# Kernel optimization log

Hardware: AMD Instinct MI355X
Metric: run time of the kernel (lower is better)

## Reference

```python
import jax, jax.numpy as jnp
import numpy as np

WS = 4           # window_size
NUM_HEADS = 4
LN_EPS = 1e-5


def setup_inputs() -> dict:
    key = jax.random.key(0)
    ks = jax.random.split(key, 8)
    d = 256
    s = 0.02
    return {
        "feature": jax.random.normal(ks[0], (8, d, 127, 127), dtype=jnp.float32),
        "ln_w": jnp.ones((d,), jnp.float32),
        "ln_b": jnp.zeros((d,), jnp.float32),
        "in_w": jax.random.normal(ks[1], (3 * d, d), jnp.float32) * s,
        "in_b": jnp.zeros((3 * d,), jnp.float32),
        "out_w": jax.random.normal(ks[2], (d, d), jnp.float32) * s,
        "out_b": jnp.zeros((d,), jnp.float32),
        "proj_w": jax.random.normal(ks[3], (d, d), jnp.float32) * s,
        "proj_b": jnp.zeros((d,), jnp.float32),
    }


def reference(feature, ln_w, ln_b, in_w, in_b, out_w, out_b, proj_w, proj_b):
    B, C, H, W = feature.shape
    ws = WS
    pad_h = (-H) % ws
    pad_w = (-W) % ws
    x = jnp.pad(feature, ((0, 0), (0, 0), (0, pad_h), (0, pad_w)))
    Hp, Wp = H + pad_h, W + pad_w
    nh, nw = Hp // ws, Wp // ws
    # NCHW -> NHWC -> windows [B*nh*nw, ws*ws, C]
    x = x.transpose(0, 2, 3, 1)
    win = (x.reshape(B, nh, ws, nw, ws, C)
            .transpose(0, 1, 3, 2, 4, 5)
            .reshape(-1, ws * ws, C))
    # LayerNorm (ddof=0, matches torch)
    mu = win.mean(-1, keepdims=True)
    var = win.var(-1, keepdims=True)
    xn = (win - mu) / jnp.sqrt(var + LN_EPS) * ln_w + ln_b
    # fused QKV projection, then split heads
    qkv = xn @ in_w.T + in_b
    q, k, v = jnp.split(qkv, 3, axis=-1)
    hd = C // NUM_HEADS
    def heads(t):
        return t.reshape(t.shape[0], t.shape[1], NUM_HEADS, hd).transpose(0, 2, 1, 3)
    q, k, v = heads(q), heads(k), heads(v)
    scores = jnp.einsum('bhqd,bhkd->bhqk', q, k) / np.float32(np.sqrt(hd))
    a = jax.nn.softmax(scores, axis=-1)
    o = jnp.einsum('bhqk,bhkd->bhqd', a, v)
    o = o.transpose(0, 2, 1, 3).reshape(-1, ws * ws, C)
    o = o @ out_w.T + out_b
    # residual + Linear + exact GELU
    y = win + jax.nn.gelu(o @ proj_w.T + proj_b, approximate=False)
    # windows -> NHWC, crop padding, -> NCHW
    y = (y.reshape(B, nh, nw, ws, ws, C)
          .transpose(0, 1, 3, 2, 4, 5)
          .reshape(B, Hp, Wp, C))
    return y[:, :H, :W, :].transpose(0, 3, 1, 2)
```

## Files before the change

kernel.cpp:

```cpp
#include <hip/hip_runtime.h>

typedef _Float16 f16;
typedef __attribute__((ext_vector_type(4))) _Float16 half4;
typedef __attribute__((ext_vector_type(8))) _Float16 half8;
typedef __attribute__((ext_vector_type(4))) float f32x4;
typedef unsigned short u16;

#define MFMA32(a,b,c) __builtin_amdgcn_mfma_f32_16x16x32_f16(a,b,c,0,0,0)
#define MFMA16(a,b,c) __builtin_amdgcn_mfma_f32_16x16x16f16(a,b,c,0,0,0)

#define W_IN0   0
#define W_OUT0  196608
#define W_PROJ0 262144
#define X0      327680
#define QK0     33882112ull
#define VT0     100990976ull

__global__ void k0_cast(const float* __restrict__ iw, const float* __restrict__ ow,
                        const float* __restrict__ pw, f16* __restrict__ W) {
    int i = blockIdx.x * 256 + threadIdx.x;
    if (i < 196608) W[W_IN0 + i] = (f16)iw[i];
    if (i < 16384) {
        const int s = i & 8191;
        const float* src = (i < 8192) ? ow : pw;
        f16* dst = W + ((i < 8192) ? W_OUT0 : W_PROJ0);
        const int r = s >> 5, sp = s & 31;
        const int u = sp ^ (r & 7);
        const int kc = u >> 2, gg = u & 3;
        const int c0 = kc * 32 + gg * 4;
        f32x4 v0 = *(const f32x4*)(src + r * 256 + c0);
        f32x4 v1 = *(const f32x4*)(src + r * 256 + c0 + 16);
        half8 o;
#pragma unroll
        for (int j = 0; j < 4; ++j) { o[j] = (f16)v0[j]; o[j + 4] = (f16)v1[j]; }
        *(half8*)(dst + (r >> 5) * 8192 + (r & 31) * 256 + sp * 8) = o;
    }
}

__global__ __launch_bounds__(256, 4)
void k1_pack(const float* __restrict__ feat, const float* __restrict__ lnw,
             const float* __restrict__ lnb, f16* __restrict__ X) {
    const int tid = threadIdx.x, lane = tid & 63, hh = tid >> 6;
    const int bid = blockIdx.x;
    const int jh = bid & 3, wi = (bid >> 2) & 31, bb = bid >> 7;
    const int h0 = wi * 4, w0 = jh * 32;
    const int wl4 = lane & 7, cg = lane >> 3;
    const int h = h0 + hh, wb = w0 + wl4 * 4;
    const bool hok = (h < 127);
    const bool edge = (wb + 3) >= 127;
    const size_t bbase = (size_t)bb * (256 * 127 * 127);
    const int c0 = cg * 32;
    const float* p0 = feat + bbase + (size_t)c0 * 16129 + (size_t)h * 127 + wb;

    half4 arr[32];
    float ss[4] = {0.f, 0.f, 0.f, 0.f}, qq[4] = {0.f, 0.f, 0.f, 0.f};
    if (hok && !edge) {
#pragma unroll
        for (int i = 0; i < 32; ++i) {
            f32x4 v = *(const f32x4*)(p0 + (size_t)i * 16129);
            half4 hv;
#pragma unroll
            for (int e = 0; e < 4; ++e) { ss[e] += v[e]; qq[e] += v[e] * v[e]; hv[e] = (f16)v[e]; }
            arr[i] = hv;
        }
    } else if (hok) {
#pragma unroll
        for (int i = 0; i < 32; ++i) {
            const float* pi = p0 + (size_t)i * 16129;
            half4 hv;
#pragma unroll
            for (int e = 0; e < 3; ++e) { float v = pi[e]; ss[e] += v; qq[e] += v * v; hv[e] = (f16)v; }
            hv[3] = (f16)0.f;
            arr[i] = hv;
        }
    } else {
#pragma unroll
        for (int i = 0; i < 32; ++i) {
            half4 hv; hv[0] = hv[1] = hv[2] = hv[3] = (f16)0.f; arr[i] = hv;
        }
    }
#pragma unroll
    for (int e = 0; e < 4; ++e) {
        ss[e] += __shfl_xor(ss[e], 8);  qq[e] += __shfl_xor(qq[e], 8);
        ss[e] += __shfl_xor(ss[e], 16); qq[e] += __shfl_xor(qq[e], 16);
        ss[e] += __shfl_xor(ss[e], 32); qq[e] += __shfl_xor(qq[e], 32);
    }
    float mu[4], rs[4];
#pragma unroll
    for (int e = 0; e < 4; ++e) {
        mu[e] = ss[e] * (1.f / 256.f);
        rs[e] = rsqrtf(qq[e] * (1.f / 256.f) - mu[e] * mu[e] + 1e-5f);
    }
#pragma unroll
    for (int q = 0; q < 4; ++q) {
        f32x4 lw0 = *(const f32x4*)(lnw + c0 + q * 8);
        f32x4 lw1 = *(const f32x4*)(lnw + c0 + q * 8 + 4);
        f32x4 lb0 = *(const f32x4*)(lnb + c0 + q * 8);
        f32x4 lb1 = *(const f32x4*)(lnb + c0 + q * 8 + 4);
#pragma unroll
        for (int e = 0; e < 4; ++e) {
            const int m = wl4 * 16 + hh * 4 + e;
            f16* xrow = X + ((size_t)bid * 128 + m) * 256 + c0;
            half8 o;
#pragma unroll
            for (int j = 0; j < 4; ++j) {
                o[j]     = (f16)(((float)arr[q * 8 + j][e]     - mu[e]) * rs[e] * lw0[j] + lb0[j]);
                o[j + 4] = (f16)(((float)arr[q * 8 + j + 4][e] - mu[e]) * rs[e] * lw1[j] + lb1[j]);
            }
            *(half8*)(xrow + q * 8) = o;
        }
    }
}

__global__ __launch_bounds__(512, 2)
void k2_qkv(const f16* __restrict__ X, const f16* __restrict__ win,
            const float* __restrict__ inb, f16* __restrict__ QK, f16* __restrict__ VT) {
    __shared__ __align__(16) char sm[49152];
    const int tid = threadIdx.x, lane = tid & 63, wv = tid >> 6;
    const int nwg = gridDim.x;
    const int bid = (blockIdx.x & 7) * (nwg >> 3) + (blockIdx.x >> 3);
    const int mt = bid / 6, nb = bid % 6;
    const size_t Mbase = (size_t)mt * 256;
    const int n0 = nb * 128;
    const int wm = wv >> 1, wn = wv & 1;
    const int c = lane & 15, g = lane >> 4;
    const int chs = (lane & 3) ^ ((lane >> 3) & 3);

    f32x4 acc[4][4];
#pragma unroll
    for (int a = 0; a < 4; ++a)
#pragma unroll
        for (int b = 0; b < 4; ++b) acc[a][b] = f32x4{0.f, 0.f, 0.f, 0.f};

    auto stage = [&](int step, int bsel) {
        const f16* As = X + Mbase * 256 + step * 32;
        const f16* Bs = win + (size_t)n0 * 256 + step * 32;
        char* base = sm + bsel * 24576;
#pragma unroll
        for (int p = 0; p < 2; ++p) {
            int row = p * 128 + wv * 16 + (lane >> 2);
            __builtin_amdgcn_global_load_lds(
                (const __attribute__((address_space(1))) unsigned int*)(As + (size_t)row * 256 + chs * 8),
                (__attribute__((address_space(3))) unsigned int*)(base + p * 8192 + wv * 1024),
                16, 0, 0);
        }
        {
            int row = wv * 16 + (lane >> 2);
            __builtin_amdgcn_global_load_lds(
                (const __attribute__((address_space(1))) unsigned int*)(Bs + (size_t)row * 256 + chs * 8),
                (__attribute__((address_space(3))) unsigned int*)(base + 16384 + wv * 1024),
                16, 0, 0);
        }
    };
    const int rsl = (g ^ ((c >> 1) & 3)) * 16;
    auto compute = [&](int bsel) {
        char* base = sm + bsel * 24576;
        half8 a[4], b[4];
#pragma unroll
        for (int mi = 0; mi < 4; ++mi) {
            int row = wm * 64 + mi * 16 + c;
            a[mi] = *(half8*)(base + row * 64 + rsl);
        }
#pragma unroll
        for (int nt = 0; nt < 4; ++nt) {
            int row = wn * 64 + nt * 16 + c;
            b[nt] = *(half8*)(base + 16384 + row * 64 + rsl);
        }
#pragma unroll
        for (int mi = 0; mi < 4; ++mi)
#pragma unroll
            for (int nt = 0; nt < 4; ++nt)
                acc[mi][nt] = MFMA32(a[mi], b[nt], acc[mi][nt]);
    };

    stage(0, 0);
    __syncthreads();
#pragma unroll
    for (int s = 0; s < 8; ++s) {
        const int bsel = s & 1;
        if (s < 7) stage(s + 1, bsel ^ 1);
        compute(bsel);
        __syncthreads();
    }

    const f32x4 z4 = {0.f, 0.f, 0.f, 0.f};
    half4 idf;
#pragma unroll
    for (int j = 0; j < 4; ++j) idf[j] = (f16)((g * 4 + j == c) ? 1.f : 0.f);

    if (n0 < 512) {
#pragma unroll
        for (int mi = 0; mi < 4; ++mi)
#pragma unroll
            for (int nt = 0; nt < 4; ++nt) {
                int n = n0 + wn * 64 + nt * 16 + c;
                float bias = inb[n];
                half4 h;
#pragma unroll
                for (int r = 0; r < 4; ++r) h[r] = (f16)(acc[mi][nt][r] + bias);
                f32x4 t = MFMA16(h, idf, z4);
                half4 o;
#pragma unroll
                for (int r = 0; r < 4; ++r) o[r] = (f16)t[r];
                size_t tok = Mbase + wm * 64 + mi * 16 + c;
                *(half4*)(QK + tok * 512 + (n0 + wn * 64 + nt * 16 + g * 4)) = o;
            }
    } else {
#pragma unroll
        for (int mi = 0; mi < 4; ++mi)
#pragma unroll
            for (int nt = 0; nt < 4; ++nt) {
                int n = n0 + wn * 64 + nt * 16 + c;
                float bias = inb[n];
                half4 h;
#pragma unroll
                for (int r = 0; r < 4; ++r) h[r] = (f16)(acc[mi][nt][r] + bias);
                int d = n - 512;
                size_t tokb = Mbase + wm * 64 + mi * 16;
                size_t winI = tokb >> 4;
                *(half4*)(VT + winI * 4096 + (size_t)d * 16 + g * 4) = h;
            }
    }
}

__global__ __launch_bounds__(256, 3)
void k3_attn(const f16* __restrict__ QK, const f16* __restrict__ VT,
             const f16* __restrict__ wout, const f16* __restrict__ wproj,
             const float* __restrict__ outb, const float* __restrict__ projb,
             f16* __restrict__ G) {
    __shared__ __align__(16) char sm[32768];
    const int tid = threadIdx.x, lane = tid & 63, wv = tid >> 6;
    const int c = lane & 15, g = lane >> 4;
    const size_t win = (size_t)blockIdx.x * 4 + wv;
    const f16* qrow = QK + (win * 16 + c) * 512;
    const f32x4 z4 = {0.f, 0.f, 0.f, 0.f};

    auto stageW = [&](const f16* img, int rc, int bsel) {
#pragma unroll
        for (int q2 = 0; q2 < 4; ++q2) {
            int ia = wv * 4 + q2;
            __builtin_amdgcn_global_load_lds(
                (const __attribute__((address_space(1))) unsigned int*)(img + rc * 8192 + ia * 512 + lane * 8),
                (__attribute__((address_space(3))) unsigned int*)(sm + bsel * 16384 + ia * 1024),
                16, 0, 0);
        }
    };

    stageW(wout, 0, 0);

    half8 ofp[4][2];
#pragma unroll
    for (int hq = 0; hq < 4; ++hq) {
        half8 af0 = *(const half8*)(qrow + 256 + hq * 64 + g * 8);
        half8 af1 = *(const half8*)(qrow + 256 + hq * 64 + 32 + g * 8);
        half8 bq0 = *(const half8*)(qrow + hq * 64 + g * 8);
        half8 bq1 = *(const half8*)(qrow + hq * 64 + 32 + g * 8);
        f32x4 sacc = MFMA32(af0, bq0, z4);
        sacc = MFMA32(af1, bq1, sacc);
        float s0 = sacc[0] * 0.125f, s1 = sacc[1] * 0.125f;
        float s2 = sacc[2] * 0.125f, s3 = sacc[3] * 0.125f;
        float mx = fmaxf(fmaxf(s0, s1), fmaxf(s2, s3));
        mx = fmaxf(mx, __shfl_xor(mx, 16));
        mx = fmaxf(mx, __shfl_xor(mx, 32));
        float p0 = __expf(s0 - mx), p1 = __expf(s1 - mx);
        float p2 = __expf(s2 - mx), p3 = __expf(s3 - mx);
        float sum = p0 + p1 + p2 + p3;
        sum += __shfl_xor(sum, 16);
        sum += __shfl_xor(sum, 32);
        float inv = 1.f / sum;
        half4 pf;
        pf[0] = (f16)(p0 * inv); pf[1] = (f16)(p1 * inv);
        pf[2] = (f16)(p2 * inv); pf[3] = (f16)(p3 * inv);
#pragma unroll
        for (int nt = 0; nt < 4; ++nt) {
            half4 vf = *(const half4*)(VT + win * 4096 + (size_t)(hq * 64 + nt * 16 + c) * 16 + g * 4);
            f32x4 o = MFMA16(vf, pf, z4);
#pragma unroll
            for (int r = 0; r < 4; ++r) ofp[hq][nt >> 1][(nt & 1) * 4 + r] = (f16)o[r];
        }
    }

    const int r0 = c, r1 = 16 + c;
    const int sw0 = (r0 & 7) << 4, sw1 = (r1 & 7) << 4;
    half8 obp[8];
    __syncthreads();

#pragma unroll
    for (int ch = 0; ch < 8; ++ch) {
        if (ch < 7) stageW(wout, ch + 1, (ch + 1) & 1);
        else        stageW(wproj, 0, (ch + 1) & 1);
        char* base = sm + (ch & 1) * 16384;
        f32x4 a0 = z4, a1 = z4;
#pragma unroll
        for (int kc = 0; kc < 8; ++kc) {
            half8 w0 = *(half8*)(base + r0 * 512 + ((kc * 64 + g * 16) ^ sw0));
            a0 = MFMA32(w0, ofp[kc >> 1][kc & 1], a0);
            half8 w1 = *(half8*)(base + r1 * 512 + ((kc * 64 + g * 16) ^ sw1));
            a1 = MFMA32(w1, ofp[kc >> 1][kc & 1], a1);
        }
        f32x4 b0 = *(const f32x4*)(outb + ch * 32 + g * 4);
        f32x4 b1 = *(const f32x4*)(outb + ch * 32 + 16 + g * 4);
#pragma unroll
        for (int r = 0; r < 4; ++r) {
            obp[ch][r]     = (f16)(a0[r] + b0[r]);
            obp[ch][4 + r] = (f16)(a1[r] + b1[r]);
        }
        __syncthreads();
    }

#pragma unroll
    for (int pc = 0; pc < 8; ++pc) {
        if (pc < 7) stageW(wproj, pc + 1, (pc + 1) & 1);
        char* base = sm + (pc & 1) * 16384;
        f32x4 a0 = z4, a1 = z4;
#pragma unroll
        for (int kc = 0; kc < 8; ++kc) {
            half8 w0 = *(half8*)(base + r0 * 512 + ((kc * 64 + g * 16) ^ sw0));
            a0 = MFMA32(w0, obp[kc], a0);
            half8 w1 = *(half8*)(base + r1 * 512 + ((kc * 64 + g * 16) ^ sw1));
            a1 = MFMA32(w1, obp[kc], a1);
        }
        f32x4 b0 = *(const f32x4*)(projb + pc * 32 + g * 4);
        f32x4 b1 = *(const f32x4*)(projb + pc * 32 + 16 + g * 4);
        half4 h0, h1;
#pragma unroll
        for (int r = 0; r < 4; ++r) {
            float x0 = a0[r] + b0[r];
            h0[r] = (f16)(0.5f * x0 * (1.f + erff(x0 * 0.70710678118f)));
            float x1 = a1[r] + b1[r];
            h1[r] = (f16)(0.5f * x1 * (1.f + erff(x1 * 0.70710678118f)));
        }
        f16* grow = G + (win * 16 + c) * 256 + pc * 32;
        *(half4*)(grow + g * 4) = h0;
        *(half4*)(grow + 16 + g * 4) = h1;
        if (pc < 7) __syncthreads();
    }
}

__global__ __launch_bounds__(256, 8)
void k4_out(const f16* __restrict__ G, const float* __restrict__ feat, float* __restrict__ outp) {
    const int tid = threadIdx.x;
    const int bid = blockIdx.x;
    const int bb = bid / 127, h = bid % 127;
    const int w = tid & 127;
    const int cq = tid >> 7;
    const bool wok = (w < 127);
    const size_t bbase = (size_t)bb * (256 * 127 * 127);
    const int wi = h >> 2, hh = h & 3;
    const int jh = w >> 5, wl4 = (w >> 2) & 7, e = w & 3;
    const size_t t = ((size_t)((bb * 32 + wi) * 4 + jh)) * 128 + wl4 * 16 + hh * 4 + e;
    const f16* gp = G + t * 256;
    const float* fp = feat + bbase + (size_t)h * 127 + w;
    float* op = outp + bbase + (size_t)h * 127 + w;
#pragma unroll 4
    for (int ci = 0; ci < 32; ++ci) {
        const int ch = ci * 8 + cq * 4;
        if (wok) {
            half4 g4 = *(const half4*)(gp + ch);
#pragma unroll
            for (int j = 0; j < 4; ++j) {
                size_t off = (size_t)(ch + j) * 16129;
                op[off] = fp[off] + (float)g4[j];
            }
        }
    }
}

extern "C" void kernel_launch(void* const* d_in, const int* in_sizes, int n_in,
                              void* d_out, int out_size, void* d_ws, size_t ws_size,
                              hipStream_t stream) {
    const float* feat   = (const float*)d_in[0];
    const float* ln_w   = (const float*)d_in[1];
    const float* ln_b   = (const float*)d_in[2];
    const float* in_w   = (const float*)d_in[3];
    const float* in_b   = (const float*)d_in[4];
    const float* out_w  = (const float*)d_in[5];
    const float* out_b  = (const float*)d_in[6];
    const float* proj_w = (const float*)d_in[7];
    const float* proj_b = (const float*)d_in[8];

    f16* W  = (f16*)d_ws;
    f16* Xb  = W + X0;
    f16* QKb = W + QK0;
    f16* VTb = W + VT0;
    f16* Gb  = Xb;

    k0_cast<<<768, 256, 0, stream>>>(in_w, out_w, proj_w, W);
    k1_pack<<<1024, 256, 0, stream>>>(feat, ln_w, ln_b, Xb);
    k2_qkv<<<3072, 512, 0, stream>>>(Xb, W + W_IN0, in_b, QKb, VTb);
    k3_attn<<<2048, 256, 0, stream>>>(QKb, VTb, W + W_OUT0, W + W_PROJ0, out_b, proj_b, Gb);
    k4_out<<<1016, 256, 0, stream>>>(Gb, feat, (float*)d_out);
}
```

Baseline: 362.0 us.

## Use 8-wave attention blocks, chunk-level XOR swizzle, and polynomial erf GELU

The attention kernel now runs 512 threads per block over 8 windows, so each staged weight chunk in LDS is shared by twice as many windows and each wave issues half as many global-to-LDS loads. The LDS swizzle moves from byte-granular XOR to 64-byte chunk-index XOR, and the weight pre-cast kernel changes to match. The library erff in GELU is replaced by the Abramowitz-Stegun polynomial with __expf, which is cheaper but carries about 1e-7 absolute error in erf. Larger blocks may reduce resident blocks per CU and add barrier cost.

```diff
diff --git a/kernel.cpp b/kernel.cpp
--- a/kernel.cpp
+++ b/kernel.cpp
@@ -15,6 +15,18 @@
 #define X0      327680
 #define QK0     33882112ull
 #define VT0     100990976ull
+
+__device__ __forceinline__ float gelu_f(float x) {
+    float z = x * 0.70710678118f;
+    float az = fabsf(z);
+    float t = 1.f / (1.f + 0.3275911f * az);
+    float e = __expf(-z * z);
+    float poly = ((((1.061405429f * t - 1.453152027f) * t + 1.421413741f) * t
+                   - 0.284496736f) * t + 0.254829592f) * t;
+    float er = 1.f - poly * e;
+    er = copysignf(er, z);
+    return 0.5f * x * (1.f + er);
+}
 
 __global__ void k0_cast(const float* __restrict__ iw, const float* __restrict__ ow,
                         const float* __restrict__ pw, f16* __restrict__ W) {
@@ -25,8 +37,8 @@
         const float* src = (i < 8192) ? ow : pw;
         f16* dst = W + ((i < 8192) ? W_OUT0 : W_PROJ0);
         const int r = s >> 5, sp = s & 31;
-        const int u = sp ^ (r & 7);
-        const int kc = u >> 2, gg = u & 3;
+        const int kc = (sp >> 2) ^ (r & 7);
+        const int gg = sp & 3;
         const int c0 = kc * 32 + gg * 4;
         f32x4 v0 = *(const f32x4*)(src + r * 256 + c0);
         f32x4 v1 = *(const f32x4*)(src + r * 256 + c0 + 16);
@@ -223,7 +235,7 @@
     }
 }
 
-__global__ __launch_bounds__(256, 3)
+__global__ __launch_bounds__(512, 2)
 void k3_attn(const f16* __restrict__ QK, const f16* __restrict__ VT,
              const f16* __restrict__ wout, const f16* __restrict__ wproj,
              const float* __restrict__ outb, const float* __restrict__ projb,
@@ -231,14 +243,14 @@
     __shared__ __align__(16) char sm[32768];
     const int tid = threadIdx.x, lane = tid & 63, wv = tid >> 6;
     const int c = lane & 15, g = lane >> 4;
-    const size_t win = (size_t)blockIdx.x * 4 + wv;
+    const size_t win = (size_t)blockIdx.x * 8 + wv;
     const f16* qrow = QK + (win * 16 + c) * 512;
     const f32x4 z4 = {0.f, 0.f, 0.f, 0.f};
 
     auto stageW = [&](const f16* img, int rc, int bsel) {
 #pragma unroll
-        for (int q2 = 0; q2 < 4; ++q2) {
-            int ia = wv * 4 + q2;
+        for (int q2 = 0; q2 < 2; ++q2) {
+            int ia = wv * 2 + q2;
             __builtin_amdgcn_global_load_lds(
                 (const __attribute__((address_space(1))) unsigned int*)(img + rc * 8192 + ia * 512 + lane * 8),
                 (__attribute__((address_space(3))) unsigned int*)(sm + bsel * 16384 + ia * 1024),
@@ -281,7 +293,7 @@
     }
 
     const int r0 = c, r1 = 16 + c;
-    const int sw0 = (r0 & 7) << 4, sw1 = (r1 & 7) << 4;
+    const int csw = c & 7;
     half8 obp[8];
     __syncthreads();
 
@@ -293,9 +305,9 @@
         f32x4 a0 = z4, a1 = z4;
 #pragma unroll
         for (int kc = 0; kc < 8; ++kc) {
-            half8 w0 = *(half8*)(base + r0 * 512 + ((kc * 64 + g * 16) ^ sw0));
+            half8 w0 = *(half8*)(base + r0 * 512 + ((kc ^ csw) * 64 + g * 16));
             a0 = MFMA32(w0, ofp[kc >> 1][kc & 1], a0);
-            half8 w1 = *(half8*)(base + r1 * 512 + ((kc * 64 + g * 16) ^ sw1));
+            half8 w1 = *(half8*)(base + r1 * 512 + ((kc ^ csw) * 64 + g * 16));
             a1 = MFMA32(w1, ofp[kc >> 1][kc & 1], a1);
         }
         f32x4 b0 = *(const f32x4*)(outb + ch * 32 + g * 4);
@@ -315,9 +327,9 @@
         f32x4 a0 = z4, a1 = z4;
 #pragma unroll
         for (int kc = 0; kc < 8; ++kc) {
-            half8 w0 = *(half8*)(base + r0 * 512 + ((kc * 64 + g * 16) ^ sw0));
+            half8 w0 = *(half8*)(base + r0 * 512 + ((kc ^ csw) * 64 + g * 16));
             a0 = MFMA32(w0, obp[kc], a0);
-            half8 w1 = *(half8*)(base + r1 * 512 + ((kc * 64 + g * 16) ^ sw1));
+            half8 w1 = *(half8*)(base + r1 * 512 + ((kc ^ csw) * 64 + g * 16));
             a1 = MFMA32(w1, obp[kc], a1);
         }
         f32x4 b0 = *(const f32x4*)(projb + pc * 32 + g * 4);
@@ -325,10 +337,8 @@
         half4 h0, h1;
 #pragma unroll
         for (int r = 0; r < 4; ++r) {
-            float x0 = a0[r] + b0[r];
-            h0[r] = (f16)(0.5f * x0 * (1.f + erff(x0 * 0.70710678118f)));
-            float x1 = a1[r] + b1[r];
-            h1[r] = (f16)(0.5f * x1 * (1.f + erff(x1 * 0.70710678118f)));
+            h0[r] = (f16)gelu_f(a0[r] + b0[r]);
+            h1[r] = (f16)gelu_f(a1[r] + b1[r]);
         }
         f16* grow = G + (win * 16 + c) * 256 + pc * 32;
         *(half4*)(grow + g * 4) = h0;
@@ -388,6 +398,6 @@
     k0_cast<<<768, 256, 0, stream>>>(in_w, out_w, proj_w, W);
     k1_pack<<<1024, 256, 0, stream>>>(feat, ln_w, ln_b, Xb);
     k2_qkv<<<3072, 512, 0, stream>>>(Xb, W + W_IN0, in_b, QKb, VTb);
-    k3_attn<<<2048, 256, 0, stream>>>(QKb, VTb, W + W_OUT0, W + W_PROJ0, out_b, proj_b, Gb);
+    k3_attn<<<1024, 512, 0, stream>>>(QKb, VTb, W + W_OUT0, W + W_PROJ0, out_b, proj_b, Gb);
     k4_out<<<1016, 256, 0, stream>>>(Gb, feat, (float*)d_out);
 }
```

Result: slower. 380.5 us (+5.1%).
